# Performance work log

Hardware: AMD Instinct MI355X
Metric: run time of the kernel (lower is better)

## Reference

```python
import jax, jax.numpy as jnp
import numpy as np

C_M = 256   # c_in (MSA channel)
C_Z = 128   # pair channel
H = 8       # no_heads
D = 32      # c_hidden per head
S = 128     # N_seq
R = 384     # N_res
INF = 1e9
LN_EPS = 1e-5


def _layer_norm(x, w, b):
    mu = jnp.mean(x, axis=-1, keepdims=True)
    var = jnp.var(x, axis=-1, keepdims=True)
    return (x - mu) * jax.lax.rsqrt(var + LN_EPS) * w + b


def setup_inputs() -> dict:
    key = jax.random.key(0)
    ks = jax.random.split(key, 10)
    s = 0.02
    return {
        "m": jax.random.normal(ks[0], (S, R, C_M), jnp.float32),
        "z": jax.random.normal(ks[1], (R, R, C_Z), jnp.float32),
        "mask": jnp.ones((S, R), jnp.float32),
        "ln_m_w": jnp.ones((C_M,), jnp.float32),
        "ln_m_b": jnp.zeros((C_M,), jnp.float32),
        "ln_z_w": jnp.ones((C_Z,), jnp.float32),
        "ln_z_b": jnp.zeros((C_Z,), jnp.float32),
        "w_z": jax.random.normal(ks[2], (C_Z, H), jnp.float32) * s,
        "w_q": jax.random.normal(ks[3], (C_M, H, D), jnp.float32) * s,
        "w_k": jax.random.normal(ks[4], (C_M, H, D), jnp.float32) * s,
        "w_v": jax.random.normal(ks[5], (C_M, H, D), jnp.float32) * s,
        "w_g": jax.random.normal(ks[6], (C_M, H, D), jnp.float32) * s,
        "b_g": jnp.zeros((H, D), jnp.float32),
        "w_o": jax.random.normal(ks[7], (H, D, C_M), jnp.float32) * s,
        "b_o": jnp.zeros((C_M,), jnp.float32),
    }


def reference(m, z, mask, ln_m_w, ln_m_b, ln_z_w, ln_z_b,
              w_z, w_q, w_k, w_v, w_g, b_g, w_o, b_o):
    # mask bias: [S, 1, 1, R]
    mask_bias = (INF * (mask - 1.0))[:, None, None, :]
    # pair bias: LN(z) -> linear to heads -> [1, H, R, R]
    z_bias = jnp.einsum("ijc,ch->hij", _layer_norm(z, ln_z_w, ln_z_b), w_z)[None]
    # LayerNorm on MSA embedding
    mn = _layer_norm(m, ln_m_w, ln_m_b)
    # q/k/v projections (no bias); q scaled by 1/sqrt(D)
    q = jnp.einsum("src,chd->srhd", mn, w_q) / np.sqrt(D).astype(np.float32)
    k = jnp.einsum("src,chd->srhd", mn, w_k)
    v = jnp.einsum("src,chd->srhd", mn, w_v)
    # logits [S, H, R, R] with additive mask and pair biases
    logits = jnp.einsum("sqhd,skhd->shqk", q, k) + mask_bias + z_bias
    a = jax.nn.softmax(logits, axis=-1)
    o = jnp.einsum("shqk,skhd->sqhd", a, v)
    # sigmoid gating from the normalized query input
    g = jax.nn.sigmoid(jnp.einsum("src,chd->srhd", mn, w_g) + b_g)
    o = o * g
    # output projection
    return jnp.einsum("srhd,hdc->src", o, w_o) + b_o
```

## Files before the change

### kernel.cpp

```cpp
#include <hip/hip_runtime.h>
#include <math.h>

#define S 128
#define R 384
#define CM 256
#define CZ 128
#define H 8
#define D 32
#define INFB 1e9f
#define LN_EPS 1e-5f
#define LOG2E 1.4426950408889634f

typedef unsigned short u16;
typedef short bf16x8 __attribute__((ext_vector_type(8)));
typedef short bf16x4 __attribute__((ext_vector_type(4)));
typedef float f32x4 __attribute__((ext_vector_type(4)));

#define NRTOT ((size_t)S * R)

__device__ inline float wave_reduce_sum(float v) {
    #pragma unroll
    for (int o = 32; o > 0; o >>= 1) v += __shfl_xor(v, o, 64);
    return v;
}

__device__ inline u16 f2bf(float f) {
    union { float f; unsigned int u; } x; x.f = f;
    unsigned int r = x.u + 0x7fffu + ((x.u >> 16) & 1u);
    return (u16)(r >> 16);
}

__device__ inline float bf2f(u16 v) {
    union { unsigned int u; float f; } x; x.u = ((unsigned int)v) << 16;
    return x.f;
}

__global__ __launch_bounds__(256) void maskprep_kernel(
    const float* __restrict__ mask, float* __restrict__ mlog) {
    int i = blockIdx.x * 256 + threadIdx.x;
    float4 mk = ((const float4*)mask)[i];
    const float MSC = INFB * LOG2E;
    float4 r;
    r.x = (mk.x - 1.0f) * MSC;
    r.y = (mk.y - 1.0f) * MSC;
    r.z = (mk.z - 1.0f) * MSC;
    r.w = (mk.w - 1.0f) * MSC;
    ((float4*)mlog)[i] = r;
}

__global__ __launch_bounds__(256) void wprep_kernel(
    const float* __restrict__ wq, const float* __restrict__ wk,
    const float* __restrict__ wv, const float* __restrict__ wg,
    const float* __restrict__ wo, u16* __restrict__ Wt) {
    int n = blockIdx.x & 255;
    int mi = blockIdx.x >> 8;
    int kc = threadIdx.x;
    const float* src = mi == 0 ? wq : mi == 1 ? wk : mi == 2 ? wv
                     : mi == 3 ? wg : wo;
    float val = src[(size_t)kc * 256 + n];
    if (mi == 0) val *= 0.17677669529663687f * LOG2E;
    size_t dst = (size_t)mi * 65536 + (size_t)(n >> 4) * 4096
               + (size_t)(kc >> 5) * 512 + (n & 15) * 32 + (kc & 31);
    Wt[dst] = f2bf(val);
}

__global__ __launch_bounds__(256) void lnm_kernel(
    const float* __restrict__ m, const float* __restrict__ lnw,
    const float* __restrict__ lnb, u16* __restrict__ A) {
    int t = threadIdx.x;
    int wave = t >> 6, lane = t & 63;
    size_t row = (size_t)blockIdx.x * 4 + wave;
    float4 x = ((const float4*)(m + row * 256))[lane];
    float ss = wave_reduce_sum(x.x + x.y + x.z + x.w);
    float sq = wave_reduce_sum(x.x * x.x + x.y * x.y + x.z * x.z + x.w * x.w);
    float mu = ss * (1.0f / 256.0f);
    float var = sq * (1.0f / 256.0f) - mu * mu;
    float rstd = rsqrtf(var + LN_EPS);
    int c = lane * 4;
    ushort4 o4;
    o4.x = f2bf((x.x - mu) * rstd * lnw[c]     + lnb[c]);
    o4.y = f2bf((x.y - mu) * rstd * lnw[c + 1] + lnb[c + 1]);
    o4.z = f2bf((x.z - mu) * rstd * lnw[c + 2] + lnb[c + 2]);
    o4.w = f2bf((x.w - mu) * rstd * lnw[c + 3] + lnb[c + 3]);
    size_t dst = (row >> 4) * 4096 + (size_t)(lane >> 3) * 512
               + (row & 15) * 32 + (lane & 7) * 4;
    *(ushort4*)(A + dst) = o4;
}

__global__ __launch_bounds__(256) void zbias_kernel(
    const float* __restrict__ z, const float* __restrict__ lnw,
    const float* __restrict__ lnb, const float* __restrict__ wz,
    float* __restrict__ zbias) {
    int t = threadIdx.x;
    int lane = t & 63, wave = t >> 6;
    int g = lane >> 4, u = lane & 15;
    int c0 = u * 8;

    float lw[8], lb[8];
    {
        float4 a = *(const float4*)(lnw + c0);
        float4 b = *(const float4*)(lnw + c0 + 4);
        lw[0]=a.x; lw[1]=a.y; lw[2]=a.z; lw[3]=a.w;
        lw[4]=b.x; lw[5]=b.y; lw[6]=b.z; lw[7]=b.w;
        float4 c = *(const float4*)(lnb + c0);
        float4 d = *(const float4*)(lnb + c0 + 4);
        lb[0]=c.x; lb[1]=c.y; lb[2]=c.z; lb[3]=c.w;
        lb[4]=d.x; lb[5]=d.y; lb[6]=d.z; lb[7]=d.w;
        #pragma unroll
        for (int i = 0; i < 8; ++i) { lw[i] *= LOG2E; lb[i] *= LOG2E; }
    }
    float uw[8][8];
    float bwp[8];
    #pragma unroll
    for (int h = 0; h < 8; ++h) bwp[h] = 0.f;
    #pragma unroll
    for (int i = 0; i < 8; ++i) {
        float4 w0 = *(const float4*)(wz + (size_t)(c0 + i) * 8);
        float4 w1 = *(const float4*)(wz + (size_t)(c0 + i) * 8 + 4);
        uw[i][0] = lw[i] * w0.x; uw[i][1] = lw[i] * w0.y;
        uw[i][2] = lw[i] * w0.z; uw[i][3] = lw[i] * w0.w;
        uw[i][4] = lw[i] * w1.x; uw[i][5] = lw[i] * w1.y;
        uw[i][6] = lw[i] * w1.z; uw[i][7] = lw[i] * w1.w;
        bwp[0] = fmaf(lb[i], w0.x, bwp[0]); bwp[1] = fmaf(lb[i], w0.y, bwp[1]);
        bwp[2] = fmaf(lb[i], w0.z, bwp[2]); bwp[3] = fmaf(lb[i], w0.w, bwp[3]);
        bwp[4] = fmaf(lb[i], w1.x, bwp[4]); bwp[5] = fmaf(lb[i], w1.y, bwp[5]);
        bwp[6] = fmaf(lb[i], w1.z, bwp[6]); bwp[7] = fmaf(lb[i], w1.w, bwp[7]);
    }

    const int nwaves = gridDim.x * 4;
    int wid = blockIdx.x * 4 + wave;
    #pragma unroll 1
    for (int it = 0; it < 4; ++it) {
        int p = (wid + it * nwaves) * 4 + g;
        const float* zp = z + (size_t)p * CZ + c0;
        float4 z0 = *(const float4*)zp;
        float4 z1 = *(const float4*)(zp + 4);
        float x[8] = {z0.x, z0.y, z0.z, z0.w, z1.x, z1.y, z1.z, z1.w};
        float ss = 0.f, sq = 0.f;
        #pragma unroll
        for (int i = 0; i < 8; ++i) { ss += x[i]; sq = fmaf(x[i], x[i], sq); }
        #pragma unroll
        for (int o = 1; o < 16; o <<= 1) {
            ss += __shfl_xor(ss, o, 64);
            sq += __shfl_xor(sq, o, 64);
        }
        float mu = ss * (1.0f / CZ);
        float var = sq * (1.0f / CZ) - mu * mu;
        float rstd = rsqrtf(var + LN_EPS);
        float ph[8];
        #pragma unroll
        for (int h = 0; h < 8; ++h) ph[h] = bwp[h];
        #pragma unroll
        for (int i = 0; i < 8; ++i) {
            float ti = (x[i] - mu) * rstd;
            #pragma unroll
            for (int h = 0; h < 8; ++h) ph[h] = fmaf(ti, uw[i][h], ph[h]);
        }
        #pragma unroll
        for (int h = 0; h < 8; ++h) {
            #pragma unroll
            for (int o = 1; o < 16; o <<= 1) ph[h] += __shfl_xor(ph[h], o, 64);
        }
        if (u < 8) {
            float outv = ph[0];
            if (u == 1) outv = ph[1];
            if (u == 2) outv = ph[2];
            if (u == 3) outv = ph[3];
            if (u == 4) outv = ph[4];
            if (u == 5) outv = ph[5];
            if (u == 6) outv = ph[6];
            if (u == 7) outv = ph[7];
            int i = p / R;
            int j = p - i * R;
            zbias[(((size_t)u * 24 + (j >> 4)) * R + i) * 16 + (j & 15)] = outv;
        }
    }
}

__global__ __launch_bounds__(512) void qkvg_gemm(
    const u16* __restrict__ A, const u16* __restrict__ Wt,
    const float* __restrict__ bg,
    u16* __restrict__ q, u16* __restrict__ k, u16* __restrict__ vT,
    u16* __restrict__ g) {
    int nb = blockIdx.y;
    size_t row0 = (size_t)blockIdx.x * 128;
    int t = threadIdx.x, lane = t & 63, wave = t >> 6;
    int l15 = lane & 15, l4 = lane >> 4;
    int wm = (wave >> 2) * 64, wn = (wave & 3) * 64;
    const u16* B = Wt + (size_t)nb * 65536;
    size_t arb = (row0 + wm) >> 4;
    int nblk = wn >> 4;
    int lelem = l15 * 32 + l4 * 8;

    f32x4 acc[4][4];
    #pragma unroll
    for (int mt = 0; mt < 4; ++mt)
        #pragma unroll
        for (int nt = 0; nt < 4; ++nt)
            acc[mt][nt] = (f32x4){0.f, 0.f, 0.f, 0.f};

    #pragma unroll
    for (int kk = 0; kk < 8; ++kk) {
        bf16x8 af[4], bfr[4];
        #pragma unroll
        for (int mt = 0; mt < 4; ++mt)
            af[mt] = *(const bf16x8*)(A + ((arb + mt) * 8 + kk) * 512 + lelem);
        #pragma unroll
        for (int nt = 0; nt < 4; ++nt)
            bfr[nt] = *(const bf16x8*)(B + ((size_t)(nblk + nt) * 8 + kk) * 512 + lelem);
        #pragma unroll
        for (int mt = 0; mt < 4; ++mt)
            #pragma unroll
            for (int nt = 0; nt < 4; ++nt)
                acc[mt][nt] = __builtin_amdgcn_mfma_f32_16x16x32_bf16(
                    af[mt], bfr[nt], acc[mt][nt], 0, 0, 0);
    }

    if (nb == 3) {
        #pragma unroll
        for (int nt = 0; nt < 4; ++nt) {
            int col = wn + nt * 16 + l15;
            int hh = col >> 5, dd = col & 31;
            float bgv = bg[col];
            #pragma unroll
            for (int mt = 0; mt < 4; ++mt)
                #pragma unroll
                for (int r = 0; r < 4; ++r) {
                    size_t row = row0 + wm + mt * 16 + l4 * 4 + r;
                    g[((size_t)hh * NRTOT + row) * 32 + dd] =
                        f2bf(1.0f / (1.0f + __expf(-(acc[mt][nt][r] + bgv))));
                }
        }
    } else if (nb == 2) {
        #pragma unroll
        for (int nt = 0; nt < 4; ++nt) {
            int col = wn + nt * 16 + l15;
            int hh = col >> 5, dd = col & 31;
            int dt = dd >> 4, d15 = dd & 15;
            #pragma unroll
            for (int mt = 0; mt < 4; ++mt) {
                size_t row = row0 + wm + mt * 16 + l4 * 4;
                int ss = (int)(row / 384);
                int rr = (int)(row - (size_t)ss * 384);
                int kb = rr >> 5;
                int k5 = rr & 31;
                int slot = ((k5 & 15) >> 2) * 8 + ((k5 & 16) ? 4 : 0);
                ushort4 pk;
                pk.x = f2bf(acc[mt][nt][0]);
                pk.y = f2bf(acc[mt][nt][1]);
                pk.z = f2bf(acc[mt][nt][2]);
                pk.w = f2bf(acc[mt][nt][3]);
                size_t off = ((((size_t)(ss * 8 + hh) * 12 + kb) * 2 + dt) * 16
                              + d15) * 32 + slot;
                *(ushort4*)(vT + off) = pk;
            }
        }
    } else {
        u16* dst = nb == 0 ? q : k;
        #pragma unroll
        for (int nt = 0; nt < 4; ++nt) {
            int col = wn + nt * 16 + l15;
            int hh = col >> 5, dd = col & 31;
            #pragma unroll
            for (int mt = 0; mt < 4; ++mt)
                #pragma unroll
                for (int r = 0; r < 4; ++r) {
                    size_t row = row0 + wm + mt * 16 + l4 * 4 + r;
                    dst[((size_t)hh * NRTOT + row) * 32 + dd] = f2bf(acc[mt][nt][r]);
                }
        }
    }
}

__global__ __launch_bounds__(512) void out_gemm(
    const u16* __restrict__ A, const u16* __restrict__ Wt,
    const float* __restrict__ bo, float* __restrict__ out) {
    size_t row0 = (size_t)blockIdx.x * 128;
    int t = threadIdx.x, lane = t & 63, wave = t >> 6;
    int l15 = lane & 15, l4 = lane >> 4;
    int wm = (wave >> 2) * 64, wn = (wave & 3) * 64;
    int nblk = wn >> 4;
    int lelem = l15 * 32 + l4 * 8;

    f32x4 acc[4][4];
    #pragma unroll
    for (int mt = 0; mt < 4; ++mt)
        #pragma unroll
        for (int nt = 0; nt < 4; ++nt)
            acc[mt][nt] = (f32x4){0.f, 0.f, 0.f, 0.f};

    #pragma unroll
    for (int kk = 0; kk < 8; ++kk) {
        bf16x8 af[4], bfr[4];
        #pragma unroll
        for (int mt = 0; mt < 4; ++mt)
            af[mt] = *(const bf16x8*)(A +
                ((size_t)kk * NRTOT + row0 + wm + mt * 16 + l15) * 32 + l4 * 8);
        #pragma unroll
        for (int nt = 0; nt < 4; ++nt)
            bfr[nt] = *(const bf16x8*)(Wt + ((size_t)(nblk + nt) * 8 + kk) * 512 + lelem);
        #pragma unroll
        for (int mt = 0; mt < 4; ++mt)
            #pragma unroll
            for (int nt = 0; nt < 4; ++nt)
                acc[mt][nt] = __builtin_amdgcn_mfma_f32_16x16x32_bf16(
                    af[mt], bfr[nt], acc[mt][nt], 0, 0, 0);
    }

    #pragma unroll
    for (int nt = 0; nt < 4; ++nt) {
        int col = wn + nt * 16 + l15;
        float bov = bo[col];
        #pragma unroll
        for (int mt = 0; mt < 4; ++mt)
            #pragma unroll
            for (int r = 0; r < 4; ++r) {
                size_t row = row0 + wm + mt * 16 + l4 * 4 + r;
                out[row * 256 + col] = acc[mt][nt][r] + bov;
            }
    }
}

__global__ __launch_bounds__(768) void attn_kernel(
    const u16* __restrict__ q, const u16* __restrict__ k,
    const u16* __restrict__ vT, const u16* __restrict__ g,
    const float* __restrict__ mlog, const float* __restrict__ zb,
    u16* __restrict__ o) {
    int h = blockIdx.x, s = blockIdx.y;
    int t = threadIdx.x;
    int lane = t & 63, wave = t >> 6;
    int l15 = lane & 15, l4 = lane >> 4;

    size_t hbase = ((size_t)h * NRTOT + (size_t)s * R) * 32;
    const u16* qh = q + hbase;
    const u16* kh = k + hbase;
    const u16* gh = g + hbase;
    u16* oh = o + hbase;
    const u16* vbase = vT + (size_t)(s * H + h) * 12 * 1024;
    const float* zbh = zb + (size_t)h * 24 * R * 16;
    const float* mrow = mlog + (size_t)s * R;

    int wq0 = wave * 32;
    bf16x8 qf[2];
    #pragma unroll
    for (int rt = 0; rt < 2; ++rt)
        qf[rt] = *(const bf16x8*)(qh + (size_t)(wq0 + rt * 16 + l15) * 32 + l4 * 8);

    bf16x8 ones;
    #pragma unroll
    for (int i = 0; i < 8; ++i) ones[i] = (short)0x3F80;

    f32x4 oacc[2][2];
    f32x4 pdacc[2];
    #pragma unroll
    for (int rt = 0; rt < 2; ++rt) {
        pdacc[rt] = (f32x4){0.f, 0.f, 0.f, 0.f};
        #pragma unroll
        for (int dt = 0; dt < 2; ++dt)
            oacc[rt][dt] = (f32x4){0.f, 0.f, 0.f, 0.f};
    }

    for (int kt = 0; kt < R; kt += 32) {
        int kb = kt >> 5;
        bf16x8 kf0 = *(const bf16x8*)(kh + (size_t)(kt + l15) * 32 + l4 * 8);
        bf16x8 kf1 = *(const bf16x8*)(kh + (size_t)(kt + 16 + l15) * 32 + l4 * 8);
        bf16x8 vb0 = *(const bf16x8*)(vbase + ((size_t)kb * 2 + 0) * 512
                                      + l15 * 32 + l4 * 8);
        bf16x8 vb1 = *(const bf16x8*)(vbase + ((size_t)kb * 2 + 1) * 512
                                      + l15 * 32 + l4 * 8);
        float4 ml0 = *(const float4*)(mrow + kt + l4 * 4);
        float4 ml1 = *(const float4*)(mrow + kt + 16 + l4 * 4);
        f32x4 zv0[2], zv1[2];
        #pragma unroll
        for (int rt = 0; rt < 2; ++rt) {
            zv0[rt] = *(const f32x4*)(zbh +
                ((size_t)(2 * kb) * R + wq0 + rt * 16 + l15) * 16 + l4 * 4);
            zv1[rt] = *(const f32x4*)(zbh +
                ((size_t)(2 * kb + 1) * R + wq0 + rt * 16 + l15) * 16 + l4 * 4);
        }

        const f32x4 z4 = {0.f, 0.f, 0.f, 0.f};
        f32x4 sf0[2], sf1[2];
        #pragma unroll
        for (int rt = 0; rt < 2; ++rt) {
            sf0[rt] = __builtin_amdgcn_mfma_f32_16x16x32_bf16(kf0, qf[rt], z4, 0, 0, 0);
            sf1[rt] = __builtin_amdgcn_mfma_f32_16x16x32_bf16(kf1, qf[rt], z4, 0, 0, 0);
        }

        #pragma unroll
        for (int rt = 0; rt < 2; ++rt) {
            float e0 = exp2f(sf0[rt][0] + ml0.x + zv0[rt][0]);
            float e1 = exp2f(sf0[rt][1] + ml0.y + zv0[rt][1]);
            float e2 = exp2f(sf0[rt][2] + ml0.z + zv0[rt][2]);
            float e3 = exp2f(sf0[rt][3] + ml0.w + zv0[rt][3]);
            float e4 = exp2f(sf1[rt][0] + ml1.x + zv1[rt][0]);
            float e5 = exp2f(sf1[rt][1] + ml1.y + zv1[rt][1]);
            float e6 = exp2f(sf1[rt][2] + ml1.z + zv1[rt][2]);
            float e7 = exp2f(sf1[rt][3] + ml1.w + zv1[rt][3]);
            bf16x8 pa;
            pa[0] = (short)(__float_as_uint(e0) >> 16);
            pa[1] = (short)(__float_as_uint(e1) >> 16);
            pa[2] = (short)(__float_as_uint(e2) >> 16);
            pa[3] = (short)(__float_as_uint(e3) >> 16);
            pa[4] = (short)(__float_as_uint(e4) >> 16);
            pa[5] = (short)(__float_as_uint(e5) >> 16);
            pa[6] = (short)(__float_as_uint(e6) >> 16);
            pa[7] = (short)(__float_as_uint(e7) >> 16);
            oacc[rt][0] = __builtin_amdgcn_mfma_f32_16x16x32_bf16(
                pa, vb0, oacc[rt][0], 0, 0, 0);
            oacc[rt][1] = __builtin_amdgcn_mfma_f32_16x16x32_bf16(
                pa, vb1, oacc[rt][1], 0, 0, 0);
            pdacc[rt] = __builtin_amdgcn_mfma_f32_16x16x32_bf16(
                pa, ones, pdacc[rt], 0, 0, 0);
        }
    }

    #pragma unroll
    for (int rt = 0; rt < 2; ++rt) {
        #pragma unroll
        for (int r = 0; r < 4; ++r) {
            float inv = 1.0f / pdacc[rt][r];
            int qrow = wq0 + rt * 16 + l4 * 4 + r;
            #pragma unroll
            for (int dt = 0; dt < 2; ++dt) {
                size_t off = (size_t)qrow * 32 + dt * 16 + l15;
                oh[off] = f2bf(oacc[rt][dt][r] * inv * bf2f(gh[off]));
            }
        }
    }
}

extern "C" void kernel_launch(void* const* d_in, const int* in_sizes, int n_in,
                              void* d_out, int out_size, void* d_ws, size_t ws_size,
                              hipStream_t stream) {
    (void)in_sizes; (void)n_in; (void)out_size; (void)ws_size;
    const float* m      = (const float*)d_in[0];
    const float* z      = (const float*)d_in[1];
    const float* mask   = (const float*)d_in[2];
    const float* ln_m_w = (const float*)d_in[3];
    const float* ln_m_b = (const float*)d_in[4];
    const float* ln_z_w = (const float*)d_in[5];
    const float* ln_z_b = (const float*)d_in[6];
    const float* w_z    = (const float*)d_in[7];
    const float* w_q    = (const float*)d_in[8];
    const float* w_k    = (const float*)d_in[9];
    const float* w_v    = (const float*)d_in[10];
    const float* w_g    = (const float*)d_in[11];
    const float* b_g    = (const float*)d_in[12];
    const float* w_o    = (const float*)d_in[13];
    const float* b_o    = (const float*)d_in[14];
    float* out = (float*)d_out;
    char* wsb = (char*)d_ws;

    const size_t NR = NRTOT;
    u16*   A    = (u16*)wsb;                     wsb += NR * 256 * 2;
    u16*   q    = (u16*)wsb;                     wsb += NR * 256 * 2;
    u16*   k    = (u16*)wsb;                     wsb += NR * 256 * 2;
    u16*   vT   = (u16*)wsb;                     wsb += NR * 256 * 2;
    u16*   o    = (u16*)wsb;                     wsb += NR * 256 * 2;
    u16*   g    = (u16*)wsb;                     wsb += NR * 256 * 2;
    float* zbp  = (float*)wsb;                   wsb += (size_t)H * R * R * 4;
    u16*   Wt   = (u16*)wsb;                     wsb += (size_t)5 * 256 * 256 * 2;
    float* mlog = (float*)wsb;                   wsb += NR * 4;

    maskprep_kernel<<<48, 256, 0, stream>>>(mask, mlog);
    wprep_kernel<<<5 * 256, 256, 0, stream>>>(w_q, w_k, w_v, w_g, w_o, Wt);
    lnm_kernel<<<NR / 4, 256, 0, stream>>>(m, ln_m_w, ln_m_b, A);
    zbias_kernel<<<2304, 256, 0, stream>>>(z, ln_z_w, ln_z_b, w_z, zbp);
    qkvg_gemm<<<dim3(NR / 128, 4), 512, 0, stream>>>(A, Wt, b_g, q, k, vT, g);
    attn_kernel<<<dim3(H, S), 768, 0, stream>>>(q, k, vT, g, mlog, zbp, o);
    out_gemm<<<NR / 128, 512, 0, stream>>>(o, Wt + (size_t)4 * 65536, b_o, out);
}
```

Baseline: 259.9 us.

## Merge prep kernels and co-schedule pair-bias LN with QKVG GEMM

The mask, weight and MSA layer-norm prep kernels become one launch that picks its branch from the block index. The z pair-bias layer norm and projection now run as extra blockIdx.y slices of the QKVG GEMM launch, so the two independent stages share one grid and can overlap. This cuts launch count and the tail gaps between kernels, at the cost of mixed-role blocks and register pressure sized for the larger branch. The softmax probabilities also switch from truncation to round-half-up when converted to bf16, which changes numerics slightly.

```diff
diff --git a/kernel.cpp b/kernel.cpp
--- a/kernel.cpp
+++ b/kernel.cpp
@@ -13,7 +13,6 @@
 
 typedef unsigned short u16;
 typedef short bf16x8 __attribute__((ext_vector_type(8)));
-typedef short bf16x4 __attribute__((ext_vector_type(4)));
 typedef float f32x4 __attribute__((ext_vector_type(4)));
 
 #define NRTOT ((size_t)S * R)
@@ -35,239 +34,239 @@
     return x.f;
 }
 
-__global__ __launch_bounds__(256) void maskprep_kernel(
-    const float* __restrict__ mask, float* __restrict__ mlog) {
-    int i = blockIdx.x * 256 + threadIdx.x;
-    float4 mk = ((const float4*)mask)[i];
-    const float MSC = INFB * LOG2E;
-    float4 r;
-    r.x = (mk.x - 1.0f) * MSC;
-    r.y = (mk.y - 1.0f) * MSC;
-    r.z = (mk.z - 1.0f) * MSC;
-    r.w = (mk.w - 1.0f) * MSC;
-    ((float4*)mlog)[i] = r;
-}
-
-__global__ __launch_bounds__(256) void wprep_kernel(
+__global__ __launch_bounds__(256) void prep_kernel(
+    const float* __restrict__ m, const float* __restrict__ lnw,
+    const float* __restrict__ lnb, u16* __restrict__ A,
     const float* __restrict__ wq, const float* __restrict__ wk,
     const float* __restrict__ wv, const float* __restrict__ wg,
-    const float* __restrict__ wo, u16* __restrict__ Wt) {
-    int n = blockIdx.x & 255;
-    int mi = blockIdx.x >> 8;
-    int kc = threadIdx.x;
-    const float* src = mi == 0 ? wq : mi == 1 ? wk : mi == 2 ? wv
-                     : mi == 3 ? wg : wo;
-    float val = src[(size_t)kc * 256 + n];
-    if (mi == 0) val *= 0.17677669529663687f * LOG2E;
-    size_t dst = (size_t)mi * 65536 + (size_t)(n >> 4) * 4096
-               + (size_t)(kc >> 5) * 512 + (n & 15) * 32 + (kc & 31);
-    Wt[dst] = f2bf(val);
-}
-
-__global__ __launch_bounds__(256) void lnm_kernel(
-    const float* __restrict__ m, const float* __restrict__ lnw,
-    const float* __restrict__ lnb, u16* __restrict__ A) {
+    const float* __restrict__ wo, u16* __restrict__ Wt,
+    const float* __restrict__ mask, float* __restrict__ mlog) {
+    int bid = blockIdx.x;
     int t = threadIdx.x;
-    int wave = t >> 6, lane = t & 63;
-    size_t row = (size_t)blockIdx.x * 4 + wave;
-    float4 x = ((const float4*)(m + row * 256))[lane];
-    float ss = wave_reduce_sum(x.x + x.y + x.z + x.w);
-    float sq = wave_reduce_sum(x.x * x.x + x.y * x.y + x.z * x.z + x.w * x.w);
-    float mu = ss * (1.0f / 256.0f);
-    float var = sq * (1.0f / 256.0f) - mu * mu;
-    float rstd = rsqrtf(var + LN_EPS);
-    int c = lane * 4;
-    ushort4 o4;
-    o4.x = f2bf((x.x - mu) * rstd * lnw[c]     + lnb[c]);
-    o4.y = f2bf((x.y - mu) * rstd * lnw[c + 1] + lnb[c + 1]);
-    o4.z = f2bf((x.z - mu) * rstd * lnw[c + 2] + lnb[c + 2]);
-    o4.w = f2bf((x.w - mu) * rstd * lnw[c + 3] + lnb[c + 3]);
-    size_t dst = (row >> 4) * 4096 + (size_t)(lane >> 3) * 512
-               + (row & 15) * 32 + (lane & 7) * 4;
-    *(ushort4*)(A + dst) = o4;
-}
-
-__global__ __launch_bounds__(256) void zbias_kernel(
+    if (bid < 12288) {
+        int wave = t >> 6, lane = t & 63;
+        size_t row = (size_t)bid * 4 + wave;
+        float4 x = ((const float4*)(m + row * 256))[lane];
+        float ss = wave_reduce_sum(x.x + x.y + x.z + x.w);
+        float sq = wave_reduce_sum(x.x * x.x + x.y * x.y + x.z * x.z + x.w * x.w);
+        float mu = ss * (1.0f / 256.0f);
+        float var = sq * (1.0f / 256.0f) - mu * mu;
+        float rstd = rsqrtf(var + LN_EPS);
+        int c = lane * 4;
+        ushort4 o4;
+        o4.x = f2bf((x.x - mu) * rstd * lnw[c]     + lnb[c]);
+        o4.y = f2bf((x.y - mu) * rstd * lnw[c + 1] + lnb[c + 1]);
+        o4.z = f2bf((x.z - mu) * rstd * lnw[c + 2] + lnb[c + 2]);
+        o4.w = f2bf((x.w - mu) * rstd * lnw[c + 3] + lnb[c + 3]);
+        size_t dst = (row >> 4) * 4096 + (size_t)(lane >> 3) * 512
+                   + (row & 15) * 32 + (lane & 7) * 4;
+        *(ushort4*)(A + dst) = o4;
+    } else if (bid < 13568) {
+        int b = bid - 12288;
+        int n = b & 255;
+        int mi = b >> 8;
+        int kc = t;
+        const float* src = mi == 0 ? wq : mi == 1 ? wk : mi == 2 ? wv
+                         : mi == 3 ? wg : wo;
+        float val = src[(size_t)kc * 256 + n];
+        if (mi == 0) val *= 0.17677669529663687f * LOG2E;
+        size_t dst = (size_t)mi * 65536 + (size_t)(n >> 4) * 4096
+                   + (size_t)(kc >> 5) * 512 + (n & 15) * 32 + (kc & 31);
+        Wt[dst] = f2bf(val);
+    } else {
+        int i = (bid - 13568) * 256 + t;
+        float4 mk = ((const float4*)mask)[i];
+        const float MSC = INFB * LOG2E;
+        float4 r;
+        r.x = (mk.x - 1.0f) * MSC;
+        r.y = (mk.y - 1.0f) * MSC;
+        r.z = (mk.z - 1.0f) * MSC;
+        r.w = (mk.w - 1.0f) * MSC;
+        ((float4*)mlog)[i] = r;
+    }
+}
+
+__global__ __launch_bounds__(512) void main_fused(
+    const u16* __restrict__ A, const u16* __restrict__ Wt,
+    const float* __restrict__ bg,
+    u16* __restrict__ q, u16* __restrict__ k, u16* __restrict__ vT,
+    u16* __restrict__ g,
     const float* __restrict__ z, const float* __restrict__ lnw,
     const float* __restrict__ lnb, const float* __restrict__ wz,
     float* __restrict__ zbias) {
-    int t = threadIdx.x;
-    int lane = t & 63, wave = t >> 6;
-    int g = lane >> 4, u = lane & 15;
-    int c0 = u * 8;
-
-    float lw[8], lb[8];
-    {
-        float4 a = *(const float4*)(lnw + c0);
-        float4 b = *(const float4*)(lnw + c0 + 4);
-        lw[0]=a.x; lw[1]=a.y; lw[2]=a.z; lw[3]=a.w;
-        lw[4]=b.x; lw[5]=b.y; lw[6]=b.z; lw[7]=b.w;
-        float4 c = *(const float4*)(lnb + c0);
-        float4 d = *(const float4*)(lnb + c0 + 4);
-        lb[0]=c.x; lb[1]=c.y; lb[2]=c.z; lb[3]=c.w;
-        lb[4]=d.x; lb[5]=d.y; lb[6]=d.z; lb[7]=d.w;
-        #pragma unroll
-        for (int i = 0; i < 8; ++i) { lw[i] *= LOG2E; lb[i] *= LOG2E; }
-    }
-    float uw[8][8];
-    float bwp[8];
-    #pragma unroll
-    for (int h = 0; h < 8; ++h) bwp[h] = 0.f;
-    #pragma unroll
-    for (int i = 0; i < 8; ++i) {
-        float4 w0 = *(const float4*)(wz + (size_t)(c0 + i) * 8);
-        float4 w1 = *(const float4*)(wz + (size_t)(c0 + i) * 8 + 4);
-        uw[i][0] = lw[i] * w0.x; uw[i][1] = lw[i] * w0.y;
-        uw[i][2] = lw[i] * w0.z; uw[i][3] = lw[i] * w0.w;
-        uw[i][4] = lw[i] * w1.x; uw[i][5] = lw[i] * w1.y;
-        uw[i][6] = lw[i] * w1.z; uw[i][7] = lw[i] * w1.w;
-        bwp[0] = fmaf(lb[i], w0.x, bwp[0]); bwp[1] = fmaf(lb[i], w0.y, bwp[1]);
-        bwp[2] = fmaf(lb[i], w0.z, bwp[2]); bwp[3] = fmaf(lb[i], w0.w, bwp[3]);
-        bwp[4] = fmaf(lb[i], w1.x, bwp[4]); bwp[5] = fmaf(lb[i], w1.y, bwp[5]);
-        bwp[6] = fmaf(lb[i], w1.z, bwp[6]); bwp[7] = fmaf(lb[i], w1.w, bwp[7]);
-    }
-
-    const int nwaves = gridDim.x * 4;
-    int wid = blockIdx.x * 4 + wave;
-    #pragma unroll 1
-    for (int it = 0; it < 4; ++it) {
-        int p = (wid + it * nwaves) * 4 + g;
-        const float* zp = z + (size_t)p * CZ + c0;
-        float4 z0 = *(const float4*)zp;
-        float4 z1 = *(const float4*)(zp + 4);
-        float x[8] = {z0.x, z0.y, z0.z, z0.w, z1.x, z1.y, z1.z, z1.w};
-        float ss = 0.f, sq = 0.f;
-        #pragma unroll
-        for (int i = 0; i < 8; ++i) { ss += x[i]; sq = fmaf(x[i], x[i], sq); }
-        #pragma unroll
-        for (int o = 1; o < 16; o <<= 1) {
-            ss += __shfl_xor(ss, o, 64);
-            sq += __shfl_xor(sq, o, 64);
-        }
-        float mu = ss * (1.0f / CZ);
-        float var = sq * (1.0f / CZ) - mu * mu;
-        float rstd = rsqrtf(var + LN_EPS);
-        float ph[8];
-        #pragma unroll
-        for (int h = 0; h < 8; ++h) ph[h] = bwp[h];
-        #pragma unroll
-        for (int i = 0; i < 8; ++i) {
-            float ti = (x[i] - mu) * rstd;
-            #pragma unroll
-            for (int h = 0; h < 8; ++h) ph[h] = fmaf(ti, uw[i][h], ph[h]);
-        }
-        #pragma unroll
-        for (int h = 0; h < 8; ++h) {
-            #pragma unroll
-            for (int o = 1; o < 16; o <<= 1) ph[h] += __shfl_xor(ph[h], o, 64);
-        }
-        if (u < 8) {
-            float outv = ph[0];
-            if (u == 1) outv = ph[1];
-            if (u == 2) outv = ph[2];
-            if (u == 3) outv = ph[3];
-            if (u == 4) outv = ph[4];
-            if (u == 5) outv = ph[5];
-            if (u == 6) outv = ph[6];
-            if (u == 7) outv = ph[7];
-            int i = p / R;
-            int j = p - i * R;
-            zbias[(((size_t)u * 24 + (j >> 4)) * R + i) * 16 + (j & 15)] = outv;
-        }
-    }
-}
-
-__global__ __launch_bounds__(512) void qkvg_gemm(
-    const u16* __restrict__ A, const u16* __restrict__ Wt,
-    const float* __restrict__ bg,
-    u16* __restrict__ q, u16* __restrict__ k, u16* __restrict__ vT,
-    u16* __restrict__ g) {
-    int nb = blockIdx.y;
-    size_t row0 = (size_t)blockIdx.x * 128;
     int t = threadIdx.x, lane = t & 63, wave = t >> 6;
     int l15 = lane & 15, l4 = lane >> 4;
-    int wm = (wave >> 2) * 64, wn = (wave & 3) * 64;
-    const u16* B = Wt + (size_t)nb * 65536;
-    size_t arb = (row0 + wm) >> 4;
-    int nblk = wn >> 4;
-    int lelem = l15 * 32 + l4 * 8;
-
-    f32x4 acc[4][4];
-    #pragma unroll
-    for (int mt = 0; mt < 4; ++mt)
-        #pragma unroll
-        for (int nt = 0; nt < 4; ++nt)
-            acc[mt][nt] = (f32x4){0.f, 0.f, 0.f, 0.f};
-
-    #pragma unroll
-    for (int kk = 0; kk < 8; ++kk) {
-        bf16x8 af[4], bfr[4];
+
+    if (blockIdx.y < 4) {
+        int nb = blockIdx.y;
+        size_t row0 = (size_t)blockIdx.x * 128;
+        int wm = (wave >> 2) * 64, wn = (wave & 3) * 64;
+        const u16* B = Wt + (size_t)nb * 65536;
+        size_t arb = (row0 + wm) >> 4;
+        int nblk = wn >> 4;
+        int lelem = l15 * 32 + l4 * 8;
+
+        f32x4 acc[4][4];
         #pragma unroll
         for (int mt = 0; mt < 4; ++mt)
-            af[mt] = *(const bf16x8*)(A + ((arb + mt) * 8 + kk) * 512 + lelem);
-        #pragma unroll
-        for (int nt = 0; nt < 4; ++nt)
-            bfr[nt] = *(const bf16x8*)(B + ((size_t)(nblk + nt) * 8 + kk) * 512 + lelem);
-        #pragma unroll
-        for (int mt = 0; mt < 4; ++mt)
             #pragma unroll
             for (int nt = 0; nt < 4; ++nt)
-                acc[mt][nt] = __builtin_amdgcn_mfma_f32_16x16x32_bf16(
-                    af[mt], bfr[nt], acc[mt][nt], 0, 0, 0);
-    }
-
-    if (nb == 3) {
-        #pragma unroll
-        for (int nt = 0; nt < 4; ++nt) {
-            int col = wn + nt * 16 + l15;
-            int hh = col >> 5, dd = col & 31;
-            float bgv = bg[col];
+                acc[mt][nt] = (f32x4){0.f, 0.f, 0.f, 0.f};
+
+        #pragma unroll
+        for (int kk = 0; kk < 8; ++kk) {
+            bf16x8 af[4], bfr[4];
             #pragma unroll
             for (int mt = 0; mt < 4; ++mt)
-                #pragma unroll
-                for (int r = 0; r < 4; ++r) {
-                    size_t row = row0 + wm + mt * 16 + l4 * 4 + r;
-                    g[((size_t)hh * NRTOT + row) * 32 + dd] =
-                        f2bf(1.0f / (1.0f + __expf(-(acc[mt][nt][r] + bgv))));
+                af[mt] = *(const bf16x8*)(A + ((arb + mt) * 8 + kk) * 512 + lelem);
+            #pragma unroll
+            for (int nt = 0; nt < 4; ++nt)
+                bfr[nt] = *(const bf16x8*)(B + ((size_t)(nblk + nt) * 8 + kk) * 512 + lelem);
+            #pragma unroll
+            for (int mt = 0; mt < 4; ++mt)
+                #pragma unroll
+                for (int nt = 0; nt < 4; ++nt)
+                    acc[mt][nt] = __builtin_amdgcn_mfma_f32_16x16x32_bf16(
+                        af[mt], bfr[nt], acc[mt][nt], 0, 0, 0);
+        }
+
+        if (nb == 3) {
+            #pragma unroll
+            for (int nt = 0; nt < 4; ++nt) {
+                int col = wn + nt * 16 + l15;
+                int hh = col >> 5, dd = col & 31;
+                float bgv = bg[col];
+                #pragma unroll
+                for (int mt = 0; mt < 4; ++mt)
+                    #pragma unroll
+                    for (int r = 0; r < 4; ++r) {
+                        size_t row = row0 + wm + mt * 16 + l4 * 4 + r;
+                        g[((size_t)hh * NRTOT + row) * 32 + dd] =
+                            f2bf(1.0f / (1.0f + __expf(-(acc[mt][nt][r] + bgv))));
+                    }
+            }
+        } else if (nb == 2) {
+            #pragma unroll
+            for (int nt = 0; nt < 4; ++nt) {
+                int col = wn + nt * 16 + l15;
+                int hh = col >> 5, dd = col & 31;
+                int dt = dd >> 4, d15 = dd & 15;
+                #pragma unroll
+                for (int mt = 0; mt < 4; ++mt) {
+                    size_t row = row0 + wm + mt * 16 + l4 * 4;
+                    int ss = (int)(row / 384);
+                    int rr = (int)(row - (size_t)ss * 384);
+                    int kb = rr >> 5;
+                    int k5 = rr & 31;
+                    int slot = ((k5 & 15) >> 2) * 8 + ((k5 & 16) ? 4 : 0);
+                    ushort4 pk;
+                    pk.x = f2bf(acc[mt][nt][0]);
+                    pk.y = f2bf(acc[mt][nt][1]);
+                    pk.z = f2bf(acc[mt][nt][2]);
+                    pk.w = f2bf(acc[mt][nt][3]);
+                    size_t off = ((((size_t)(ss * 8 + hh) * 12 + kb) * 2 + dt) * 16
+                                  + d15) * 32 + slot;
+                    *(ushort4*)(vT + off) = pk;
                 }
-        }
-    } else if (nb == 2) {
-        #pragma unroll
-        for (int nt = 0; nt < 4; ++nt) {
-            int col = wn + nt * 16 + l15;
-            int hh = col >> 5, dd = col & 31;
-            int dt = dd >> 4, d15 = dd & 15;
-            #pragma unroll
-            for (int mt = 0; mt < 4; ++mt) {
-                size_t row = row0 + wm + mt * 16 + l4 * 4;
-                int ss = (int)(row / 384);
-                int rr = (int)(row - (size_t)ss * 384);
-                int kb = rr >> 5;
-                int k5 = rr & 31;
-                int slot = ((k5 & 15) >> 2) * 8 + ((k5 & 16) ? 4 : 0);
-                ushort4 pk;
-                pk.x = f2bf(acc[mt][nt][0]);
-                pk.y = f2bf(acc[mt][nt][1]);
-                pk.z = f2bf(acc[mt][nt][2]);
-                pk.w = f2bf(acc[mt][nt][3]);
-                size_t off = ((((size_t)(ss * 8 + hh) * 12 + kb) * 2 + dt) * 16
-                              + d15) * 32 + slot;
-                *(ushort4*)(vT + off) = pk;
+            }
+        } else {
+            u16* dst = nb == 0 ? q : k;
+            #pragma unroll
+            for (int nt = 0; nt < 4; ++nt) {
+                int col = wn + nt * 16 + l15;
+                int hh = col >> 5, dd = col & 31;
+                #pragma unroll
+                for (int mt = 0; mt < 4; ++mt)
+                    #pragma unroll
+                    for (int r = 0; r < 4; ++r) {
+                        size_t row = row0 + wm + mt * 16 + l4 * 4 + r;
+                        dst[((size_t)hh * NRTOT + row) * 32 + dd] = f2bf(acc[mt][nt][r]);
+                    }
             }
         }
     } else {
-        u16* dst = nb == 0 ? q : k;
-        #pragma unroll
-        for (int nt = 0; nt < 4; ++nt) {
-            int col = wn + nt * 16 + l15;
-            int hh = col >> 5, dd = col & 31;
-            #pragma unroll
-            for (int mt = 0; mt < 4; ++mt)
-                #pragma unroll
-                for (int r = 0; r < 4; ++r) {
-                    size_t row = row0 + wm + mt * 16 + l4 * 4 + r;
-                    dst[((size_t)hh * NRTOT + row) * 32 + dd] = f2bf(acc[mt][nt][r]);
-                }
+        int gidx = lane >> 4, u = lane & 15;
+        int c0 = u * 8;
+
+        float lw[8], lb[8];
+        {
+            float4 a = *(const float4*)(lnw + c0);
+            float4 b = *(const float4*)(lnw + c0 + 4);
+            lw[0]=a.x; lw[1]=a.y; lw[2]=a.z; lw[3]=a.w;
+            lw[4]=b.x; lw[5]=b.y; lw[6]=b.z; lw[7]=b.w;
+            float4 c = *(const float4*)(lnb + c0);
+            float4 d = *(const float4*)(lnb + c0 + 4);
+            lb[0]=c.x; lb[1]=c.y; lb[2]=c.z; lb[3]=c.w;
+            lb[4]=d.x; lb[5]=d.y; lb[6]=d.z; lb[7]=d.w;
+            #pragma unroll
+            for (int i = 0; i < 8; ++i) { lw[i] *= LOG2E; lb[i] *= LOG2E; }
+        }
+        float uw[8][8];
+        float bwp[8];
+        #pragma unroll
+        for (int h = 0; h < 8; ++h) bwp[h] = 0.f;
+        #pragma unroll
+        for (int i = 0; i < 8; ++i) {
+            float4 w0 = *(const float4*)(wz + (size_t)(c0 + i) * 8);
+            float4 w1 = *(const float4*)(wz + (size_t)(c0 + i) * 8 + 4);
+            uw[i][0] = lw[i] * w0.x; uw[i][1] = lw[i] * w0.y;
+            uw[i][2] = lw[i] * w0.z; uw[i][3] = lw[i] * w0.w;
+            uw[i][4] = lw[i] * w1.x; uw[i][5] = lw[i] * w1.y;
+            uw[i][6] = lw[i] * w1.z; uw[i][7] = lw[i] * w1.w;
+            bwp[0] = fmaf(lb[i], w0.x, bwp[0]); bwp[1] = fmaf(lb[i], w0.y, bwp[1]);
+            bwp[2] = fmaf(lb[i], w0.z, bwp[2]); bwp[3] = fmaf(lb[i], w0.w, bwp[3]);
+            bwp[4] = fmaf(lb[i], w1.x, bwp[4]); bwp[5] = fmaf(lb[i], w1.y, bwp[5]);
+            bwp[6] = fmaf(lb[i], w1.z, bwp[6]); bwp[7] = fmaf(lb[i], w1.w, bwp[7]);
+        }
+
+        int zbid = (blockIdx.y - 4) * 384 + blockIdx.x;
+        int wid = zbid * 8 + wave;
+        const int nwaves = 9216;
+        #pragma unroll 1
+        for (int it = 0; it < 4; ++it) {
+            int p = (wid + it * nwaves) * 4 + gidx;
+            const float* zp = z + (size_t)p * CZ + c0;
+            float4 z0 = *(const float4*)zp;
+            float4 z1 = *(const float4*)(zp + 4);
+            float x[8] = {z0.x, z0.y, z0.z, z0.w, z1.x, z1.y, z1.z, z1.w};
+            float ss = 0.f, sq = 0.f;
+            #pragma unroll
+            for (int i = 0; i < 8; ++i) { ss += x[i]; sq = fmaf(x[i], x[i], sq); }
+            #pragma unroll
+            for (int o = 1; o < 16; o <<= 1) {
+                ss += __shfl_xor(ss, o, 64);
+                sq += __shfl_xor(sq, o, 64);
+            }
+            float mu = ss * (1.0f / CZ);
+            float var = sq * (1.0f / CZ) - mu * mu;
+            float rstd = rsqrtf(var + LN_EPS);
+            float ph[8];
+            #pragma unroll
+            for (int h = 0; h < 8; ++h) ph[h] = bwp[h];
+            #pragma unroll
+            for (int i = 0; i < 8; ++i) {
+                float ti = (x[i] - mu) * rstd;
+                #pragma unroll
+                for (int h = 0; h < 8; ++h) ph[h] = fmaf(ti, uw[i][h], ph[h]);
+            }
+            #pragma unroll
+            for (int h = 0; h < 8; ++h) {
+                #pragma unroll
+                for (int o = 1; o < 16; o <<= 1) ph[h] += __shfl_xor(ph[h], o, 64);
+            }
+            if (u < 8) {
+                float outv = ph[0];
+                if (u == 1) outv = ph[1];
+                if (u == 2) outv = ph[2];
+                if (u == 3) outv = ph[3];
+                if (u == 4) outv = ph[4];
+                if (u == 5) outv = ph[5];
+                if (u == 6) outv = ph[6];
+                if (u == 7) outv = ph[7];
+                int i = p / R;
+                int j = p - i * R;
+                zbias[(((size_t)u * 24 + (j >> 4)) * R + i) * 16 + (j & 15)] = outv;
+            }
         }
     }
 }
@@ -398,14 +397,14 @@
             float e6 = exp2f(sf1[rt][2] + ml1.z + zv1[rt][2]);
             float e7 = exp2f(sf1[rt][3] + ml1.w + zv1[rt][3]);
             bf16x8 pa;
-            pa[0] = (short)(__float_as_uint(e0) >> 16);
-            pa[1] = (short)(__float_as_uint(e1) >> 16);
-            pa[2] = (short)(__float_as_uint(e2) >> 16);
-            pa[3] = (short)(__float_as_uint(e3) >> 16);
-            pa[4] = (short)(__float_as_uint(e4) >> 16);
-            pa[5] = (short)(__float_as_uint(e5) >> 16);
-            pa[6] = (short)(__float_as_uint(e6) >> 16);
-            pa[7] = (short)(__float_as_uint(e7) >> 16);
+            pa[0] = (short)((__float_as_uint(e0) + 0x8000u) >> 16);
+            pa[1] = (short)((__float_as_uint(e1) + 0x8000u) >> 16);
+            pa[2] = (short)((__float_as_uint(e2) + 0x8000u) >> 16);
+            pa[3] = (short)((__float_as_uint(e3) + 0x8000u) >> 16);
+            pa[4] = (short)((__float_as_uint(e4) + 0x8000u) >> 16);
+            pa[5] = (short)((__float_as_uint(e5) + 0x8000u) >> 16);
+            pa[6] = (short)((__float_as_uint(e6) + 0x8000u) >> 16);
+            pa[7] = (short)((__float_as_uint(e7) + 0x8000u) >> 16);
             oacc[rt][0] = __builtin_amdgcn_mfma_f32_16x16x32_bf16(
                 pa, vb0, oacc[rt][0], 0, 0, 0);
             oacc[rt][1] = __builtin_amdgcn_mfma_f32_16x16x32_bf16(
@@ -463,11 +462,11 @@
     u16*   Wt   = (u16*)wsb;                     wsb += (size_t)5 * 256 * 256 * 2;
     float* mlog = (float*)wsb;                   wsb += NR * 4;
 
-    maskprep_kernel<<<48, 256, 0, stream>>>(mask, mlog);
-    wprep_kernel<<<5 * 256, 256, 0, stream>>>(w_q, w_k, w_v, w_g, w_o, Wt);
-    lnm_kernel<<<NR / 4, 256, 0, stream>>>(m, ln_m_w, ln_m_b, A);
-    zbias_kernel<<<2304, 256, 0, stream>>>(z, ln_z_w, ln_z_b, w_z, zbp);
-    qkvg_gemm<<<dim3(NR / 128, 4), 512, 0, stream>>>(A, Wt, b_g, q, k, vT, g);
+    prep_kernel<<<13616, 256, 0, stream>>>(m, ln_m_w, ln_m_b, A,
+                                           w_q, w_k, w_v, w_g, w_o, Wt,
+                                           mask, mlog);
+    main_fused<<<dim3(384, 7), 512, 0, stream>>>(A, Wt, b_g, q, k, vT, g,
+                                                 z, ln_z_w, ln_z_b, w_z, zbp);
     attn_kernel<<<dim3(H, S), 768, 0, stream>>>(q, k, vT, g, mlog, zbp, o);
     out_gemm<<<NR / 128, 512, 0, stream>>>(o, Wt + (size_t)4 * 65536, b_o, out);
 }
```

Result: faster. 248.6 us (-4.3%).
